# Kernel optimization log

Hardware: AMD Instinct MI355X
Metric: run time of the kernel (lower is better)

Reference implementation:

```python
import jax, jax.numpy as jnp
import numpy as np

NUM_HEADS = 16
LN_EPS = 1e-12


def setup_inputs() -> dict:
    key = jax.random.key(0)
    ks = jax.random.split(key, 4)
    L, B, D = 2048, 2, 1024
    x = jax.random.normal(ks[0], (L, B, D), dtype=jnp.float32)
    attention_mask = jax.random.randint(ks[1], (B, L), 0, 2, dtype=jnp.int32)
    ln_w = jnp.ones((D,), dtype=jnp.float32)
    ln_b = jnp.zeros((D,), dtype=jnp.float32)
    qkv_w = jax.random.normal(ks[2], (3 * D, D), dtype=jnp.float32) * 0.02
    qkv_b = jnp.zeros((3 * D,), dtype=jnp.float32)
    out_w = jax.random.normal(ks[3], (D, D), dtype=jnp.float32) * 0.02
    out_b = jnp.zeros((D,), dtype=jnp.float32)
    return {"x": x, "attention_mask": attention_mask, "ln_w": ln_w, "ln_b": ln_b,
            "qkv_w": qkv_w, "qkv_b": qkv_b, "out_w": out_w, "out_b": out_b}


def _layer_norm(x, w, b):
    mu = jnp.mean(x, axis=-1, keepdims=True)
    var = jnp.mean(jnp.square(x - mu), axis=-1, keepdims=True)
    return (x - mu) * jax.lax.rsqrt(var + LN_EPS) * w + b


def reference(x, attention_mask, ln_w, ln_b, qkv_w, qkv_b, out_w, out_b):
    L, B, D = x.shape
    H = NUM_HEADS
    hd = D // H
    scale = 1.0 / np.sqrt(hd).astype(np.float32)

    xn = _layer_norm(x, ln_w, ln_b)                       # (L, B, D)
    qkv = xn @ qkv_w.T + qkv_b                            # (L, B, 3D)
    q, k, v = jnp.split(qkv, 3, axis=-1)
    # (L, B, D) -> (L, B*H, hd) -> (B*H, L, hd)
    q = q.reshape(L, B * H, hd).swapaxes(0, 1)
    k = k.reshape(L, B * H, hd).swapaxes(0, 1)
    v = v.reshape(L, B * H, hd).swapaxes(0, 1)

    scores = jnp.einsum('nld,nmd->nlm', q, k) * scale     # (B*H, L, L)
    mask = jnp.broadcast_to(attention_mask[:, None, :], (B, H, L)).reshape(B * H, 1, L)
    scores = jnp.where(mask == 0, -jnp.inf, scores)
    probs = jax.nn.softmax(scores, axis=-1)               # masked cols -> 0
    # dropout prob = 0.0 -> identity
    context = jnp.einsum('nlm,nmd->nld', probs, v)        # (B*H, L, hd)
    context = context.swapaxes(0, 1).reshape(L, B, D)
    return context @ out_w.T + out_b
```

## Files before the change

kernel.cpp:

```cpp
#include <hip/hip_runtime.h>
#include <hip/hip_bf16.h>
#include <cstdint>

static constexpr int LSEQ = 2048;
static constexpr int BB   = 2;
static constexpr int DM   = 1024;
static constexpr int NHD  = 16;
static constexpr int HD   = 64;
static constexpr int ROWS = LSEQ * BB;
static constexpr int NQKV = 3 * DM;

typedef __attribute__((ext_vector_type(8))) short v8s;
typedef __attribute__((ext_vector_type(4))) float v4f;

#if __has_builtin(__builtin_amdgcn_exp2f)
#define EXP2F(x) __builtin_amdgcn_exp2f(x)
#else
#define EXP2F(x) __expf((x) * 0.69314718056f)
#endif

static constexpr float QSCALE = 0.125f * 1.44269504089f;
static constexpr float NEGM   = -10.0f * 1.44269504089f;

__device__ __forceinline__ unsigned short f2bf(float f) {
    unsigned int u = __builtin_bit_cast(unsigned int, f);
    u += 0x7fffu + ((u >> 16) & 1u);
    return (unsigned short)(u >> 16);
}

__device__ __forceinline__ void gload_lds16(const void* g, void* l) {
    auto gp = (const __attribute__((address_space(1))) unsigned int*)(uintptr_t)g;
    auto lp = (__attribute__((address_space(3))) unsigned int*)(uintptr_t)l;
    __builtin_amdgcn_global_load_lds(gp, lp, 16, 0, 0);
}

__global__ __launch_bounds__(256) void cast_w_kernel(const float* __restrict__ qkv_w,
                                                     const float* __restrict__ out_w,
                                                     unsigned short* __restrict__ wq,
                                                     unsigned short* __restrict__ wo) {
    size_t i = ((size_t)blockIdx.x * 256 + threadIdx.x) * 8;
    const float* src; unsigned short* dst; size_t off;
    if (i < (size_t)NQKV * DM) { src = qkv_w; dst = wq; off = i; }
    else                       { src = out_w; dst = wo; off = i - (size_t)NQKV * DM; }
    float4 a = *(const float4*)(src + off);
    float4 b = *(const float4*)(src + off + 4);
    ushort4 o0, o1;
    o0.x = f2bf(a.x); o0.y = f2bf(a.y); o0.z = f2bf(a.z); o0.w = f2bf(a.w);
    o1.x = f2bf(b.x); o1.y = f2bf(b.y); o1.z = f2bf(b.z); o1.w = f2bf(b.w);
    *(ushort4*)(dst + off)     = o0;
    *(ushort4*)(dst + off + 4) = o1;
}

__global__ __launch_bounds__(256) void ln_cast_kernel(const float* __restrict__ x,
                                                      const float* __restrict__ w,
                                                      const float* __restrict__ bia,
                                                      unsigned short* __restrict__ xn) {
    const int row = blockIdx.x;
    const int t = threadIdx.x;
    const float* xr = x + (size_t)row * DM;
    float4 v = ((const float4*)xr)[t];
    float s  = v.x + v.y + v.z + v.w;
    float sq = v.x*v.x + v.y*v.y + v.z*v.z + v.w*v.w;
    #pragma unroll
    for (int off = 32; off > 0; off >>= 1) {
        s  += __shfl_down(s, off);
        sq += __shfl_down(sq, off);
    }
    __shared__ float red[8];
    const int wv = t >> 6;
    if ((t & 63) == 0) { red[wv] = s; red[4 + wv] = sq; }
    __syncthreads();
    if (t == 0) {
        float S = red[0] + red[1] + red[2] + red[3];
        float Q = red[4] + red[5] + red[6] + red[7];
        float mu  = S * (1.0f / DM);
        float var = Q * (1.0f / DM) - mu * mu;
        red[0] = mu;
        red[1] = rsqrtf(var + 1e-12f);
    }
    __syncthreads();
    const float mu = red[0], rs = red[1];
    float4 wv4 = ((const float4*)w)[t];
    float4 bv4 = ((const float4*)bia)[t];
    ushort4 o;
    o.x = f2bf((v.x - mu) * rs * wv4.x + bv4.x);
    o.y = f2bf((v.y - mu) * rs * wv4.y + bv4.y);
    o.z = f2bf((v.z - mu) * rs * wv4.z + bv4.z);
    o.w = f2bf((v.w - mu) * rs * wv4.w + bv4.w);
    ((ushort4*)(xn + (size_t)row * DM))[t] = o;
}

template <int BN, int EPI>
__global__ __launch_bounds__(512) void gemm2_kernel(const unsigned short* __restrict__ A,
                                                    const unsigned short* __restrict__ Bt,
                                                    const float* __restrict__ bias,
                                                    float* __restrict__ outF,
                                                    unsigned short* __restrict__ qb,
                                                    unsigned short* __restrict__ kb,
                                                    unsigned short* __restrict__ vt,
                                                    int N) {
    constexpr int K  = DM;
    constexpr int FC = BN / 64;
    constexpr int WN = BN / 4;
    constexpr int NT = K / 64;
    __shared__ unsigned short Al[2][256 * 64];
    __shared__ unsigned short Bl[2][BN * 64];
    const int nbn = N / BN;
    const int bm = blockIdx.x / nbn;
    const int bn = blockIdx.x % nbn;
    const int tid = threadIdx.x;
    const int w = tid >> 6, lane = tid & 63;
    const int l15 = lane & 15, l4 = lane >> 4;
    const int wm = w >> 2, wn = w & 3;
    const unsigned short* Ab = A  + (size_t)bm * 256 * K;
    const unsigned short* Bb = Bt + (size_t)bn * BN * K;
    const int srow8  = lane >> 3;
    const int schunk = ((lane & 7) ^ (srow8 & 7)) * 8;
    const int swz    = l15 & 7;

    v4f acc[8][FC] = {};

    auto STAGE = [&](int buf, int t) {
        const int k0 = t * 64;
        #pragma unroll
        for (int i = 0; i < 4; ++i) {
            const int r0 = i * 64 + w * 8;
            gload_lds16(Ab + (size_t)(r0 + srow8) * K + k0 + schunk, &Al[buf][r0 * 64]);
        }
        #pragma unroll
        for (int i = 0; i < BN / 64; ++i) {
            const int r0 = i * 64 + w * 8;
            gload_lds16(Bb + (size_t)(r0 + srow8) * K + k0 + schunk, &Bl[buf][r0 * 64]);
        }
    };
    auto COMPUTE = [&](int buf) {
        #pragma unroll
        for (int ks = 0; ks < 2; ++ks) {
            v8s af[8]; v8s bf[FC];
            #pragma unroll
            for (int m = 0; m < 8; ++m) {
                const int row = wm * 128 + m * 16 + l15;
                af[m] = *(const v8s*)&Al[buf][row * 64 + ((ks * 4 + l4) ^ swz) * 8];
            }
            #pragma unroll
            for (int n = 0; n < FC; ++n) {
                const int row = wn * WN + n * 16 + l15;
                bf[n] = *(const v8s*)&Bl[buf][row * 64 + ((ks * 4 + l4) ^ swz) * 8];
            }
            #pragma unroll
            for (int m = 0; m < 8; ++m)
                #pragma unroll
                for (int n = 0; n < FC; ++n)
                    acc[m][n] = __builtin_amdgcn_mfma_f32_16x16x32_bf16(af[m], bf[n], acc[m][n], 0, 0, 0);
        }
    };

    STAGE(0, 0);
    __syncthreads();
    int cur = 0;
    for (int t = 0; t < NT - 1; ++t) {
        STAGE(cur ^ 1, t + 1);
        COMPUTE(cur);
        __syncthreads();
        cur ^= 1;
    }
    COMPUTE(cur);

    #pragma unroll
    for (int m = 0; m < 8; ++m) {
        #pragma unroll
        for (int n = 0; n < FC; ++n) {
            #pragma unroll
            for (int r = 0; r < 4; ++r) {
                const int row = bm * 256 + wm * 128 + m * 16 + l4 * 4 + r;
                const int col = bn * BN + wn * WN + n * 16 + l15;
                const float val = acc[m][n][r] + bias[col];
                if (EPI == 0) {
                    outF[(size_t)row * N + col] = val;
                } else {
                    const int lq = row >> 1, b = row & 1;
                    const int which = col >> 10, jr = col & 1023;
                    const int h = jr >> 6, d = jr & 63;
                    const int bh = b * NHD + h;
                    if (which == 0)      qb[((size_t)bh * LSEQ + lq) * HD + d] = f2bf(val * QSCALE);
                    else if (which == 1) kb[((size_t)bh * LSEQ + lq) * HD + d] = f2bf(val);
                    else                 vt[((size_t)bh * HD + d) * LSEQ + lq] = f2bf(val);
                }
            }
        }
    }
}

__global__ __launch_bounds__(256) void attn_kernel(const unsigned short* __restrict__ qbuf,
                                                   const unsigned short* __restrict__ kbuf,
                                                   const unsigned short* __restrict__ vtbuf,
                                                   const int* __restrict__ amask,
                                                   unsigned short* __restrict__ ctx) {
    __shared__ unsigned short Kl[2][64 * 64];
    __shared__ unsigned short Vl[2][64 * 64];
    __shared__ unsigned short Pl[4][2][16 * 72];
    __shared__ float mb_all[LSEQ];
    const int id = blockIdx.x;
    const int inner = id >> 3;
    const int bh = (id & 7) * 4 + (inner & 3);
    const int qblk = inner >> 2;
    const int b = bh >> 4, h = bh & 15;
    const int tid = threadIdx.x;
    const int w = tid >> 6, lane = tid & 63;
    const int l15 = lane & 15, l4 = lane >> 4;
    const int q0 = qblk * 128 + w * 32;

    #pragma unroll
    for (int i = 0; i < LSEQ / 256; ++i)
        mb_all[i * 256 + tid] = amask[b * LSEQ + i * 256 + tid] ? NEGM : -1e30f;

    v8s qf[2][2];
    #pragma unroll
    for (int qt = 0; qt < 2; ++qt) {
        const unsigned short* Qp = qbuf + ((size_t)bh * LSEQ + q0 + qt * 16 + l15) * HD + l4 * 8;
        qf[qt][0] = *(const v8s*)Qp;
        qf[qt][1] = *(const v8s*)(Qp + 32);
    }
    const unsigned short* Kb = kbuf  + (size_t)bh * LSEQ * HD;
    const unsigned short* Vb = vtbuf + (size_t)bh * HD * LSEQ;

    v4f O[2][4] = {};
    float lsum[2][4] = {};

    const int srow = lane >> 3;
    const int schunk = ((lane & 7) ^ srow) * 8;
    const int swz = l15 & 7;

    auto STAGE = [&](int buf, int kv0) {
        const int r0 = w * 16;
        gload_lds16(Kb + (size_t)(kv0 + r0 + srow) * HD + schunk,       &Kl[buf][r0 * 64]);
        gload_lds16(Kb + (size_t)(kv0 + r0 + 8 + srow) * HD + schunk,   &Kl[buf][(r0 + 8) * 64]);
        gload_lds16(Vb + (size_t)(r0 + srow) * LSEQ + kv0 + schunk,     &Vl[buf][r0 * 64]);
        gload_lds16(Vb + (size_t)(r0 + 8 + srow) * LSEQ + kv0 + schunk, &Vl[buf][(r0 + 8) * 64]);
    };

    STAGE(0, 0);
    __syncthreads();
    int cur = 0;
    for (int t = 0; t < LSEQ / 64; ++t) {
        if (t + 1 < LSEQ / 64) STAGE(cur ^ 1, (t + 1) * 64);
        const int kv0 = t * 64;

        v8s kf[4][2];
        float mb[4];
        #pragma unroll
        for (int n = 0; n < 4; ++n) {
            const int krow = n * 16 + l15;
            kf[n][0] = *(const v8s*)&Kl[cur][krow * 64 + ((0 + l4) ^ swz) * 8];
            kf[n][1] = *(const v8s*)&Kl[cur][krow * 64 + ((4 + l4) ^ swz) * 8];
            mb[n] = mb_all[kv0 + krow];
        }

        #pragma unroll
        for (int qt = 0; qt < 2; ++qt) {
            unsigned short* Pw = Pl[w][qt];
            #pragma unroll
            for (int n = 0; n < 4; ++n) {
                v4f a = {};
                a = __builtin_amdgcn_mfma_f32_16x16x32_bf16(qf[qt][0], kf[n][0], a, 0, 0, 0);
                a = __builtin_amdgcn_mfma_f32_16x16x32_bf16(qf[qt][1], kf[n][1], a, 0, 0, 0);
                #pragma unroll
                for (int r = 0; r < 4; ++r) {
                    const float p = EXP2F(a[r] + mb[n]);
                    lsum[qt][r] += p;
                    unsigned int u = __builtin_bit_cast(unsigned int, p) + 0x8000u;
                    Pw[(l4 * 4 + r) * 72 + n * 16 + l15] = (unsigned short)(u >> 16);
                }
            }
        }
        asm volatile("s_waitcnt lgkmcnt(0)" ::: "memory");
        __builtin_amdgcn_sched_barrier(0);

        #pragma unroll
        for (int ks = 0; ks < 2; ++ks) {
            const v8s pa0 = *(const v8s*)&Pl[w][0][l15 * 72 + ks * 32 + l4 * 8];
            const v8s pa1 = *(const v8s*)&Pl[w][1][l15 * 72 + ks * 32 + l4 * 8];
            #pragma unroll
            for (int n = 0; n < 4; ++n) {
                const int vrow = n * 16 + l15;
                const v8s vf = *(const v8s*)&Vl[cur][vrow * 64 + ((ks * 4 + l4) ^ swz) * 8];
                O[0][n] = __builtin_amdgcn_mfma_f32_16x16x32_bf16(pa0, vf, O[0][n], 0, 0, 0);
                O[1][n] = __builtin_amdgcn_mfma_f32_16x16x32_bf16(pa1, vf, O[1][n], 0, 0, 0);
            }
        }
        __syncthreads();
        cur ^= 1;
    }

    #pragma unroll
    for (int qt = 0; qt < 2; ++qt)
        #pragma unroll
        for (int r = 0; r < 4; ++r) {
            #pragma unroll
            for (int off = 1; off < 16; off <<= 1)
                lsum[qt][r] += __shfl_xor(lsum[qt][r], off);
        }

    #pragma unroll
    for (int qt = 0; qt < 2; ++qt) {
        float inv[4];
        #pragma unroll
        for (int r = 0; r < 4; ++r) inv[r] = 1.0f / lsum[qt][r];
        #pragma unroll
        for (int n = 0; n < 4; ++n) {
            #pragma unroll
            for (int r = 0; r < 4; ++r) {
                const int lq = q0 + qt * 16 + l4 * 4 + r;
                const float val = O[qt][n][r] * inv[r];
                ctx[((size_t)lq * BB + b) * DM + h * HD + n * 16 + l15] = f2bf(val);
            }
        }
    }
}

extern "C" void kernel_launch(void* const* d_in, const int* in_sizes, int n_in,
                              void* d_out, int out_size, void* d_ws, size_t ws_size,
                              hipStream_t stream) {
    (void)in_sizes; (void)n_in; (void)out_size; (void)ws_size;
    const float* x     = (const float*)d_in[0];
    const int*   amask = (const int*)d_in[1];
    const float* ln_w  = (const float*)d_in[2];
    const float* ln_b  = (const float*)d_in[3];
    const float* qkv_w = (const float*)d_in[4];
    const float* qkv_b = (const float*)d_in[5];
    const float* out_w = (const float*)d_in[6];
    const float* out_b = (const float*)d_in[7];
    float* out = (float*)d_out;

    unsigned short* ws    = (unsigned short*)d_ws;
    unsigned short* xn    = ws;
    unsigned short* wq    = xn + (size_t)ROWS * DM;
    unsigned short* wo    = wq + (size_t)NQKV * DM;
    unsigned short* qbuf  = wo + (size_t)DM * DM;
    unsigned short* kbuf  = qbuf + (size_t)BB * NHD * LSEQ * HD;
    unsigned short* vtbuf = kbuf + (size_t)BB * NHD * LSEQ * HD;
    unsigned short* ctx   = vtbuf + (size_t)BB * NHD * LSEQ * HD;

    cast_w_kernel<<<2048, 256, 0, stream>>>(qkv_w, out_w, wq, wo);
    ln_cast_kernel<<<ROWS, 256, 0, stream>>>(x, ln_w, ln_b, xn);
    gemm2_kernel<192, 1><<<(ROWS / 256) * (NQKV / 192), 512, 0, stream>>>(
        xn, wq, qkv_b, nullptr, qbuf, kbuf, vtbuf, NQKV);
    attn_kernel<<<512, 256, 0, stream>>>(qbuf, kbuf, vtbuf, amask, ctx);
    gemm2_kernel<128, 0><<<(ROWS / 256) * (DM / 128), 512, 0, stream>>>(
        ctx, wo, out_b, out, nullptr, nullptr, nullptr, DM);
}
```

Measured before the change: 143.5 us.

## Switch attention to 32x32x16 MFMA with register-resident P via lane shuffles

```diff
diff --git a/kernel.cpp b/kernel.cpp
--- a/kernel.cpp
+++ b/kernel.cpp
@@ -10,8 +10,10 @@
 static constexpr int ROWS = LSEQ * BB;
 static constexpr int NQKV = 3 * DM;
 
-typedef __attribute__((ext_vector_type(8))) short v8s;
-typedef __attribute__((ext_vector_type(4))) float v4f;
+typedef __attribute__((ext_vector_type(8)))  short v8s;
+typedef __attribute__((ext_vector_type(4)))  float v4f;
+typedef __attribute__((ext_vector_type(16))) float v16f;
+typedef __attribute__((ext_vector_type(4)))  unsigned int v4u;
 
 #if __has_builtin(__builtin_amdgcn_exp2f)
 #define EXP2F(x) __builtin_amdgcn_exp2f(x)
@@ -198,38 +200,36 @@
                                                    unsigned short* __restrict__ ctx) {
     __shared__ unsigned short Kl[2][64 * 64];
     __shared__ unsigned short Vl[2][64 * 64];
-    __shared__ unsigned short Pl[4][2][16 * 72];
-    __shared__ float mb_all[LSEQ];
+    __shared__ alignas(16) float mb_all[LSEQ];
+    __shared__ alignas(16) float inv_l[4 * 32];
     const int id = blockIdx.x;
     const int inner = id >> 3;
     const int bh = (id & 7) * 4 + (inner & 3);
     const int qblk = inner >> 2;
-    const int b = bh >> 4, h = bh & 15;
+    const int bat = bh >> 4, h = bh & 15;
     const int tid = threadIdx.x;
     const int w = tid >> 6, lane = tid & 63;
-    const int l15 = lane & 15, l4 = lane >> 4;
+    const int l31 = lane & 31, hi = lane >> 5;
     const int q0 = qblk * 128 + w * 32;
 
     #pragma unroll
     for (int i = 0; i < LSEQ / 256; ++i)
-        mb_all[i * 256 + tid] = amask[b * LSEQ + i * 256 + tid] ? NEGM : -1e30f;
-
-    v8s qf[2][2];
-    #pragma unroll
-    for (int qt = 0; qt < 2; ++qt) {
-        const unsigned short* Qp = qbuf + ((size_t)bh * LSEQ + q0 + qt * 16 + l15) * HD + l4 * 8;
-        qf[qt][0] = *(const v8s*)Qp;
-        qf[qt][1] = *(const v8s*)(Qp + 32);
-    }
+        mb_all[i * 256 + tid] = amask[bat * LSEQ + i * 256 + tid] ? NEGM : -1e30f;
+
+    const unsigned short* Qp = qbuf + ((size_t)bh * LSEQ + q0 + l31) * HD + hi * 8;
+    v8s qfr[4];
+    #pragma unroll
+    for (int s = 0; s < 4; ++s) qfr[s] = *(const v8s*)(Qp + s * 16);
+
     const unsigned short* Kb = kbuf  + (size_t)bh * LSEQ * HD;
     const unsigned short* Vb = vtbuf + (size_t)bh * HD * LSEQ;
 
-    v4f O[2][4] = {};
-    float lsum[2][4] = {};
+    v16f O0 = {}, O1 = {};
+    float lsum = 0.f;
 
     const int srow = lane >> 3;
     const int schunk = ((lane & 7) ^ srow) * 8;
-    const int swz = l15 & 7;
+    const int rsw = l31 & 7;
 
     auto STAGE = [&](int buf, int kv0) {
         const int r0 = w * 16;
@@ -246,74 +246,73 @@
         if (t + 1 < LSEQ / 64) STAGE(cur ^ 1, (t + 1) * 64);
         const int kv0 = t * 64;
 
-        v8s kf[4][2];
-        float mb[4];
-        #pragma unroll
-        for (int n = 0; n < 4; ++n) {
-            const int krow = n * 16 + l15;
-            kf[n][0] = *(const v8s*)&Kl[cur][krow * 64 + ((0 + l4) ^ swz) * 8];
-            kf[n][1] = *(const v8s*)&Kl[cur][krow * 64 + ((4 + l4) ^ swz) * 8];
-            mb[n] = mb_all[kv0 + krow];
-        }
-
-        #pragma unroll
-        for (int qt = 0; qt < 2; ++qt) {
-            unsigned short* Pw = Pl[w][qt];
-            #pragma unroll
-            for (int n = 0; n < 4; ++n) {
-                v4f a = {};
-                a = __builtin_amdgcn_mfma_f32_16x16x32_bf16(qf[qt][0], kf[n][0], a, 0, 0, 0);
-                a = __builtin_amdgcn_mfma_f32_16x16x32_bf16(qf[qt][1], kf[n][1], a, 0, 0, 0);
+        #pragma unroll
+        for (int kvh = 0; kvh < 2; ++kvh) {
+            v16f sc = {};
+            #pragma unroll
+            for (int s = 0; s < 4; ++s) {
+                const v8s kf = *(const v8s*)&Kl[cur][(kvh * 32 + l31) * 64 + ((2 * s + hi) ^ rsw) * 8];
+                sc = __builtin_amdgcn_mfma_f32_32x32x16_bf16(kf, qfr[s], sc, 0, 0, 0);
+            }
+            float4 mbv[4];
+            #pragma unroll
+            for (int g = 0; g < 4; ++g)
+                mbv[g] = *(const float4*)&mb_all[kv0 + kvh * 32 + g * 8 + hi * 4];
+            float pf[16];
+            #pragma unroll
+            for (int g = 0; g < 4; ++g) {
                 #pragma unroll
-                for (int r = 0; r < 4; ++r) {
-                    const float p = EXP2F(a[r] + mb[n]);
-                    lsum[qt][r] += p;
-                    unsigned int u = __builtin_bit_cast(unsigned int, p) + 0x8000u;
-                    Pw[(l4 * 4 + r) * 72 + n * 16 + l15] = (unsigned short)(u >> 16);
+                for (int bq = 0; bq < 4; ++bq) {
+                    const float mbx = (bq == 0) ? mbv[g].x : (bq == 1) ? mbv[g].y
+                                     : (bq == 2) ? mbv[g].z : mbv[g].w;
+                    const float p = EXP2F(sc[g * 4 + bq] + mbx);
+                    pf[g * 4 + bq] = p;
+                    lsum += p;
                 }
             }
-        }
-        asm volatile("s_waitcnt lgkmcnt(0)" ::: "memory");
-        __builtin_amdgcn_sched_barrier(0);
-
-        #pragma unroll
-        for (int ks = 0; ks < 2; ++ks) {
-            const v8s pa0 = *(const v8s*)&Pl[w][0][l15 * 72 + ks * 32 + l4 * 8];
-            const v8s pa1 = *(const v8s*)&Pl[w][1][l15 * 72 + ks * 32 + l4 * 8];
-            #pragma unroll
-            for (int n = 0; n < 4; ++n) {
-                const int vrow = n * 16 + l15;
-                const v8s vf = *(const v8s*)&Vl[cur][vrow * 64 + ((ks * 4 + l4) ^ swz) * 8];
-                O[0][n] = __builtin_amdgcn_mfma_f32_16x16x32_bf16(pa0, vf, O[0][n], 0, 0, 0);
-                O[1][n] = __builtin_amdgcn_mfma_f32_16x16x32_bf16(pa1, vf, O[1][n], 0, 0, 0);
+            #pragma unroll
+            for (int c = 0; c < 2; ++c) {
+                unsigned int W[4];
+                #pragma unroll
+                for (int k = 0; k < 4; ++k)
+                    asm("v_cvt_pk_bf16_f32 %0, %1, %2"
+                        : "=v"(W[k]) : "v"(pf[8 * c + 2 * k]), "v"(pf[8 * c + 2 * k + 1]));
+                const unsigned int sel0 = hi ? W[0] : W[2];
+                const unsigned int sel1 = hi ? W[1] : W[3];
+                const unsigned int S0 = (unsigned int)__shfl_xor((int)sel0, 32);
+                const unsigned int S1 = (unsigned int)__shfl_xor((int)sel1, 32);
+                v4u fw;
+                fw.x = hi ? S0 : W[0];
+                fw.y = hi ? S1 : W[1];
+                fw.z = hi ? W[2] : S0;
+                fw.w = hi ? W[3] : S1;
+                const v8s pa = __builtin_bit_cast(v8s, fw);
+                const int vch = (kvh * 4 + c * 2 + hi);
+                const v8s vf0 = *(const v8s*)&Vl[cur][(l31) * 64      + (vch ^ rsw) * 8];
+                const v8s vf1 = *(const v8s*)&Vl[cur][(32 + l31) * 64 + (vch ^ rsw) * 8];
+                O0 = __builtin_amdgcn_mfma_f32_32x32x16_bf16(pa, vf0, O0, 0, 0, 0);
+                O1 = __builtin_amdgcn_mfma_f32_32x32x16_bf16(pa, vf1, O1, 0, 0, 0);
             }
         }
         __syncthreads();
         cur ^= 1;
     }
 
-    #pragma unroll
-    for (int qt = 0; qt < 2; ++qt)
-        #pragma unroll
-        for (int r = 0; r < 4; ++r) {
-            #pragma unroll
-            for (int off = 1; off < 16; off <<= 1)
-                lsum[qt][r] += __shfl_xor(lsum[qt][r], off);
-        }
-
-    #pragma unroll
-    for (int qt = 0; qt < 2; ++qt) {
-        float inv[4];
-        #pragma unroll
-        for (int r = 0; r < 4; ++r) inv[r] = 1.0f / lsum[qt][r];
-        #pragma unroll
-        for (int n = 0; n < 4; ++n) {
-            #pragma unroll
-            for (int r = 0; r < 4; ++r) {
-                const int lq = q0 + qt * 16 + l4 * 4 + r;
-                const float val = O[qt][n][r] * inv[r];
-                ctx[((size_t)lq * BB + b) * DM + h * HD + n * 16 + l15] = f2bf(val);
-            }
+    lsum += __shfl_xor(lsum, 32);
+    if (hi == 0) inv_l[w * 32 + l31] = 1.0f / lsum;
+    asm volatile("s_waitcnt lgkmcnt(0)" ::: "memory");
+    __builtin_amdgcn_sched_barrier(0);
+
+    #pragma unroll
+    for (int g = 0; g < 4; ++g) {
+        const float4 iv = *(const float4*)&inv_l[w * 32 + g * 8 + hi * 4];
+        #pragma unroll
+        for (int bq = 0; bq < 4; ++bq) {
+            const float ivx = (bq == 0) ? iv.x : (bq == 1) ? iv.y : (bq == 2) ? iv.z : iv.w;
+            const int lq = q0 + g * 8 + hi * 4 + bq;
+            unsigned short* crow = ctx + ((size_t)lq * BB + bat) * DM + h * HD;
+            crow[l31]      = f2bf(O0[g * 4 + bq] * ivx);
+            crow[32 + l31] = f2bf(O1[g * 4 + bq] * ivx);
         }
     }
 }
```

Result: faster. 132.9 us (-7.4%).
